# Kernel tuning notes

Measured on AMD Instinct MI355X. Metric: run time of the kernel, lower is better.

The kernel has to match this reference:

```python
import jax, jax.numpy as jnp
import numpy as np

B, S, D = 4, 2048, 1024
E, K, I = 8, 2, 2752  # num_experts, top_k, intermediate_size (64*ceil(1024*8/3/64))


def setup_inputs() -> dict:
    key = jax.random.key(0)
    k0, k1, k2, k3, k4 = jax.random.split(key, 5)
    return {
        "x": jax.random.normal(k0, (B, S, D), jnp.float32),
        "router_w": jax.random.normal(k1, (D, E), jnp.float32) * 0.02,   # gate Linear, no bias
        "w_gate": jax.random.normal(k2, (E, D, I), jnp.float32) * 0.02,  # per-expert gate proj
        "w_up": jax.random.normal(k3, (E, D, I), jnp.float32) * 0.02,    # per-expert up proj
        "w_down": jax.random.normal(k4, (E, I, D), jnp.float32) * 0.02,  # per-expert down proj
    }


def reference(x, router_w, w_gate, w_up, w_down):
    orig_shape = x.shape
    d = orig_shape[-1]
    xf = x.reshape(-1, d)                      # [T, D]
    T = xf.shape[0]
    n_experts = router_w.shape[1]

    # Router: softmax over all experts, then top-k and renormalize (matches torch order).
    probs = jax.nn.softmax(xf @ router_w, axis=-1)        # [T, E]
    w, idx = jax.lax.top_k(probs, K)                       # [T, K]
    w = w / (jnp.sum(w, axis=-1, keepdims=True) + 1e-6)

    # Dense combine weights: combine[t, e] = routing weight of expert e for token t (0 if unrouted).
    combine = jnp.zeros((T, n_experts), xf.dtype).at[jnp.arange(T)[:, None], idx].add(w)

    # Per-expert GatedMLP (SwiGLU, no bias, dropout=0 in eval): Down(SiLU(Gate(x)) * Up(x)).
    out = jnp.zeros_like(xf)
    for e in range(n_experts):  # fixed small expert count; data dims stay vectorized
        h = jax.nn.silu(xf @ w_gate[e]) * (xf @ w_up[e])   # [T, I]
        out = out + combine[:, e:e + 1] * (h @ w_down[e])  # scatter-combine
    return out.reshape(orig_shape)
```

## Files before the change

kernel.cpp:

```cpp
#include <hip/hip_runtime.h>
#include <hip/hip_bf16.h>
#include <math.h>

#define T_TOKENS 8192
#define D_MODEL  1024
#define N_EXP    8
#define I_RAW    2752
#define I_PAD    2816
#define N_CAT    5632
#define MAXROWS  18432
#define NYT      72
#define DUMP_SID (2 * T_TOKENS)

typedef __attribute__((ext_vector_type(8))) short bf16x8;
typedef __attribute__((ext_vector_type(8))) unsigned short ushort8;
typedef __attribute__((ext_vector_type(4))) float f32x4;
typedef unsigned short ushort_t;

#define CTRL_COUNT 0
#define CTRL_CUR   8
#define CTRL_SEG   16
#define CTRL_YT    32

#define VMW(n)  asm volatile("s_waitcnt vmcnt(" n ")" ::: "memory")
#define BARRIER() asm volatile("s_barrier" ::: "memory")

__device__ __forceinline__ void gll16(const void* g, void* l) {
  __builtin_amdgcn_global_load_lds(
      (const __attribute__((address_space(1))) void*)g,
      (__attribute__((address_space(3))) void*)l, 16, 0, 0);
}

__device__ __forceinline__ float silu_mul(float g, float u) {
  return g / (1.f + __expf(-g)) * u;
}

__device__ __forceinline__ float bf2f(ushort_t u) {
  return __uint_as_float((unsigned)u << 16);
}

__global__ void __launch_bounds__(64) router_kernel(
    const float* __restrict__ x, const float* __restrict__ rw,
    int* __restrict__ topidx, float* __restrict__ topw,
    __hip_bfloat16* __restrict__ xb) {
  const int t = blockIdx.x;
  const int lane = threadIdx.x;
  const float4* xr4 = (const float4*)(x + (size_t)t * D_MODEL);
  __hip_bfloat16* xbr = xb + (size_t)t * D_MODEL;
  float acc[N_EXP];
#pragma unroll
  for (int e = 0; e < N_EXP; ++e) acc[e] = 0.f;
#pragma unroll
  for (int i = 0; i < 4; ++i) {
    const int f4 = i * 64 + lane;
    const float4 v = xr4[f4];
    const int d0 = f4 * 4;
    const float* r = rw + (size_t)d0 * N_EXP;
#pragma unroll
    for (int e = 0; e < N_EXP; ++e)
      acc[e] = fmaf(v.x, r[e], fmaf(v.y, r[N_EXP + e],
               fmaf(v.z, r[2 * N_EXP + e], fmaf(v.w, r[3 * N_EXP + e], acc[e]))));
    __hip_bfloat16 b0 = __float2bfloat16(v.x), b1 = __float2bfloat16(v.y);
    __hip_bfloat16 b2 = __float2bfloat16(v.z), b3 = __float2bfloat16(v.w);
    ushort4 o;
    o.x = *(ushort_t*)&b0; o.y = *(ushort_t*)&b1;
    o.z = *(ushort_t*)&b2; o.w = *(ushort_t*)&b3;
    *(ushort4*)&xbr[d0] = o;
  }
#pragma unroll
  for (int e = 0; e < N_EXP; ++e) {
    for (int off = 32; off > 0; off >>= 1) acc[e] += __shfl_xor(acc[e], off, 64);
  }
  if (lane == 0) {
    float m = acc[0];
#pragma unroll
    for (int e = 1; e < N_EXP; ++e) m = fmaxf(m, acc[e]);
    float p[N_EXP], s = 0.f;
#pragma unroll
    for (int e = 0; e < N_EXP; ++e) { p[e] = expf(acc[e] - m); s += p[e]; }
    int i0 = 0; float v0 = p[0];
#pragma unroll
    for (int e = 1; e < N_EXP; ++e) if (p[e] > v0) { v0 = p[e]; i0 = e; }
    int i1 = -1; float v1 = -1.f;
#pragma unroll
    for (int e = 0; e < N_EXP; ++e) if (e != i0 && p[e] > v1) { v1 = p[e]; i1 = e; }
    v0 /= s; v1 /= s;
    const float r = v0 + v1 + 1e-6f;
    v0 /= r; v1 /= r;
    topidx[t * 2] = i0; topidx[t * 2 + 1] = i1;
    topw[t * 2] = v0;  topw[t * 2 + 1] = v1;
  }
}

__global__ void __launch_bounds__(512) hist_kernel(
    const int* __restrict__ topidx, int* __restrict__ ctrl) {
  __shared__ int lh[N_EXP];
  const int tid = threadIdx.x;
  if (tid < N_EXP) lh[tid] = 0;
  __syncthreads();
  const int g = blockIdx.x * 512 + tid;
  atomicAdd(&lh[topidx[g]], 1);
  __syncthreads();
  if (tid < N_EXP) atomicAdd(&ctrl[CTRL_COUNT + tid], lh[tid]);
}

__global__ void __launch_bounds__(256) transpose_cvt_kernel(
    const float* __restrict__ in, __hip_bfloat16* __restrict__ out,
    int Rin, int Cin, int Co, long in_es, long out_es, int mode) {
  __shared__ float tile[64][65];
  const float* inp = in + (size_t)blockIdx.z * in_es;
  __hip_bfloat16* outp = out + (size_t)blockIdx.z * out_es;
  const int b0 = blockIdx.x * 64;
  const int a0 = blockIdx.y * 64;
  const int tid = threadIdx.x;
  const bool inb = (b0 < Rin) && (a0 < Cin);
  const int bi0 = tid >> 4, a4 = (tid & 15) * 4;
  if (inb) {
#pragma unroll
    for (int i = 0; i < 4; ++i) {
      const int bi = bi0 + i * 16;
      const float4 v = *(const float4*)&inp[(size_t)(b0 + bi) * Cin + a0 + a4];
      tile[bi][a4] = v.x; tile[bi][a4 + 1] = v.y;
      tile[bi][a4 + 2] = v.z; tile[bi][a4 + 3] = v.w;
    }
  } else {
#pragma unroll
    for (int i = 0; i < 4; ++i) {
      const int bi = bi0 + i * 16;
      tile[bi][a4] = 0.f; tile[bi][a4 + 1] = 0.f;
      tile[bi][a4 + 2] = 0.f; tile[bi][a4 + 3] = 0.f;
    }
  }
  __syncthreads();
#pragma unroll
  for (int half = 0; half < 2; ++half) {
    const int g = tid + half * 256;
    const int al = g >> 3, bc = (g & 7) * 8;
    ushort8 o;
#pragma unroll
    for (int j = 0; j < 8; ++j) {
      __hip_bfloat16 h = __float2bfloat16(tile[bc + j][al]);
      o[j] = *(const ushort_t*)&h;
    }
    const int a = a0 + al;
    int A;
    if (mode == 0) A = a;
    else A = ((a >> 5) << 6) + ((mode == 2) ? 32 : 0) + (a & 31);
    *(ushort8*)&outp[(size_t)A * Co + b0 + bc] = o;
  }
}

__global__ void padfill_kernel(int* __restrict__ rowmap, float* __restrict__ roww) {
  const int i = blockIdx.x * blockDim.x + threadIdx.x;
  if (i < MAXROWS) { rowmap[i] = DUMP_SID; roww[i] = 0.f; }
}

__global__ void scan_kernel(int* __restrict__ ctrl) {
  if (threadIdx.x == 0 && blockIdx.x == 0) {
    int s = 0, yt = 0;
    ctrl[CTRL_SEG] = 0;
    for (int e = 0; e < N_EXP; ++e) {
      const int c = ctrl[CTRL_COUNT + e];
      const int padded = (c + 255) & ~255;
      const int n = padded >> 8;
      for (int j = 0; j < n; ++j) ctrl[CTRL_YT + yt + j] = e;
      yt += n;
      s += padded;
      ctrl[CTRL_SEG + 1 + e] = s;
    }
    for (; yt < NYT; ++yt) ctrl[CTRL_YT + yt] = -1;
  }
}

__global__ void __launch_bounds__(512) scatter_kernel(
    const int* __restrict__ topidx, const float* __restrict__ topw,
    int* __restrict__ ctrl, int* __restrict__ rowmap,
    float* __restrict__ roww) {
  __shared__ int lh[N_EXP];
  __shared__ int lbase[N_EXP];
  const int tid = threadIdx.x;
  if (tid < N_EXP) lh[tid] = 0;
  __syncthreads();
  const int g = blockIdx.x * 512 + tid;
  const int e = topidx[g];
  const int rank = atomicAdd(&lh[e], 1);
  __syncthreads();
  if (tid < N_EXP) lbase[tid] = atomicAdd(&ctrl[CTRL_CUR + tid], lh[tid]);
  __syncthreads();
  const int pos = ctrl[CTRL_SEG + e] + lbase[e] + rank;
  rowmap[pos] = g;
  roww[pos] = topw[g];
}

__global__ void __launch_bounds__(512, 2) gemm1_kernel(
    const __hip_bfloat16* __restrict__ xb,
    const __hip_bfloat16* __restrict__ wcat,
    __hip_bfloat16* __restrict__ H,
    const int* __restrict__ rowmap, const float* __restrict__ roww,
    const int* __restrict__ ctrl) {
  const unsigned b = blockIdx.x;
  const int xcd = b & 7;
  const unsigned w = b >> 3;
  const int yt = xcd * 9 + (int)(w % 9);
  const int xn = (int)(w / 9);
  const int e = ctrl[CTRL_YT + yt];
  if (e < 0) return;
  const int row0 = yt * 256;
  const int nbase = xn * 256;
  const int tid = threadIdx.x, lane = tid & 63, wid = tid >> 6;
  const int wrm = (wid >> 2) * 128, wrn = (wid & 3) * 64;

  __shared__ __align__(16) __hip_bfloat16 sA[2][2][8192];
  __shared__ __align__(16) __hip_bfloat16 sB[2][2][8192];
  __shared__ float sW[256];

  if (tid < 256) sW[tid] = roww[row0 + tid];

  const int srow = tid >> 2;
  const int kc = ((tid & 3) - ((tid >> 3) & 3)) & 3;
  int tok0 = rowmap[row0 + srow] >> 1;
  int tok1 = rowmap[row0 + 128 + srow] >> 1;
  tok0 = min(tok0, T_TOKENS - 1);
  tok1 = min(tok1, T_TOKENS - 1);
  const __hip_bfloat16* gA0 = xb + (size_t)tok0 * D_MODEL + kc * 8;
  const __hip_bfloat16* gA1 = xb + (size_t)tok1 * D_MODEL + kc * 8;
  const __hip_bfloat16* gB0 = wcat + ((size_t)e * N_CAT + nbase + srow) * D_MODEL + kc * 8;
  const __hip_bfloat16* gB1 = gB0 + (size_t)128 * D_MODEL;

  __syncthreads();

  auto stageA = [&](int sl_, int kh, int kt) {
    const int ko = kt * 64 + kh * 32;
    gll16(gA0 + ko, &sA[sl_][kh][tid * 8]);
    gll16(gA1 + ko, &sA[sl_][kh][4096 + tid * 8]);
  };
  auto stageB = [&](int sl_, int kh, int kt) {
    const int ko = kt * 64 + kh * 32;
    gll16(gB0 + ko, &sB[sl_][kh][tid * 8]);
    gll16(gB1 + ko, &sB[sl_][kh][4096 + tid * 8]);
  };

  f32x4 acc[8][4];
  const f32x4 z4 = {0.f, 0.f, 0.f, 0.f};
#pragma unroll
  for (int a_ = 0; a_ < 8; ++a_)
#pragma unroll
    for (int b_ = 0; b_ < 4; ++b_) acc[a_][b_] = z4;

  const int poff = ((lane >> 4) + ((lane & 15) >> 1)) & 3;
  const int arow = (wrm + (lane & 15)) * 32 + poff * 8;
  const int brow = (wrn + (lane & 15)) * 32 + poff * 8;

  const int NT = D_MODEL / 64;
  stageA(0, 0, 0); stageB(0, 0, 0);
  stageA(0, 1, 0); stageB(0, 1, 0);
  stageA(1, 0, 1); stageB(1, 0, 1);

#define G1_PHASE(SL, KH, STG)                                                  \
  {                                                                            \
    VMW("8");                                                                  \
    BARRIER();                                                                 \
    bf16x8 af[8], bfv[4];                                                      \
    _Pragma("unroll")                                                          \
    for (int mi = 0; mi < 8; ++mi)                                             \
      af[mi] = *(const bf16x8*)&sA[SL][KH][arow + mi * 512];                   \
    _Pragma("unroll")                                                          \
    for (int ni = 0; ni < 4; ++ni)                                             \
      bfv[ni] = *(const bf16x8*)&sB[SL][KH][brow + ni * 512];                  \
    STG;                                                                       \
    __builtin_amdgcn_s_setprio(1);                                             \
    _Pragma("unroll")                                                          \
    for (int mi = 0; mi < 8; ++mi)                                             \
      _Pragma("unroll")                                                        \
      for (int ni = 0; ni < 4; ++ni)                                           \
        acc[mi][ni] = __builtin_amdgcn_mfma_f32_16x16x32_bf16(af[mi], bfv[ni], acc[mi][ni], 0, 0, 0); \
    __builtin_amdgcn_s_setprio(0);                                             \
    BARRIER();                                                                 \
  }

#define G1_KTILE(SL, T)                                                        \
  {                                                                            \
    const int tn1 = ((T) + 1 < NT) ? (T) + 1 : 0;                              \
    const int tn2 = ((T) + 2 < NT) ? (T) + 2 : 0;                              \
    G1_PHASE(SL, 0, stageA(1 - (SL), 1, tn1); stageB(1 - (SL), 1, tn1))        \
    G1_PHASE(SL, 1, stageA((SL), 0, tn2);     stageB((SL), 0, tn2))            \
  }

  for (int t = 0; t < NT; t += 2) {
    G1_KTILE(0, t)
    G1_KTILE(1, t + 1)
  }
  VMW("0");

  const int hcolbase = ((nbase + wrn) >> 6) * 32;
#pragma unroll
  for (int mi = 0; mi < 8; ++mi) {
    const int r0 = wrm + mi * 16 + ((lane >> 4) * 4);
#pragma unroll
    for (int ni = 0; ni < 2; ++ni) {
      const int hcol = hcolbase + ni * 16 + (lane & 15);
      const f32x4 g = acc[mi][ni], u = acc[mi][ni + 2];
#pragma unroll
      for (int j = 0; j < 4; ++j) {
        const float h = silu_mul(g[j], u[j]) * sW[r0 + j];
        H[(size_t)(row0 + r0 + j) * I_PAD + hcol] = __float2bfloat16(h);
      }
    }
  }
}

__global__ void __launch_bounds__(256, 4) gemm2_kernel(
    const __hip_bfloat16* __restrict__ H,
    const __hip_bfloat16* __restrict__ wdt,
    ushort_t* __restrict__ slot,
    const int* __restrict__ rowmap, const int* __restrict__ ctrl) {
  const unsigned b = blockIdx.x;
  const int xcd = b & 7;
  const unsigned w = b >> 3;
  const int mt = xcd * 18 + (int)(w % 18);
  const int xn = (int)(w / 18);
  const int e = ctrl[CTRL_YT + (mt >> 1)];
  if (e < 0) return;
  const int row0 = mt * 128;
  const int nbase = xn * 128;
  const int tid = threadIdx.x, lane = tid & 63, wid = tid >> 6;
  const int wr = (wid >> 1) * 64, wc = (wid & 1) * 64;

  __shared__ __align__(16) __hip_bfloat16 sA[128 * 64];
  __shared__ __align__(16) __hip_bfloat16 sB[128 * 64];
  __shared__ int sTok[128];

  if (tid < 128) sTok[tid] = rowmap[row0 + tid];

  const __hip_bfloat16* gA[4];
  const __hip_bfloat16* gB[4];
#pragma unroll
  for (int i = 0; i < 4; ++i) {
    const int c = i * 256 + tid;
    const int row = c >> 3;
    const int kc8 = ((c & 7) - row) & 7;
    gA[i] = H + (size_t)(row0 + row) * I_PAD + kc8 * 8;
    gB[i] = wdt + ((size_t)e * D_MODEL + nbase + row) * I_PAD + kc8 * 8;
  }

  f32x4 acc[4][4];
  const f32x4 z4 = {0.f, 0.f, 0.f, 0.f};
#pragma unroll
  for (int a_ = 0; a_ < 4; ++a_)
#pragma unroll
    for (int b_ = 0; b_ < 4; ++b_) acc[a_][b_] = z4;

  const int NT = I_PAD / 64;
  for (int kt = 0; kt < NT; ++kt) {
    __syncthreads();
#pragma unroll
    for (int i = 0; i < 4; ++i) {
      const int c = i * 256 + tid;
      gll16(gA[i] + kt * 64, &sA[c * 8]);
      gll16(gB[i] + kt * 64, &sB[c * 8]);
    }
    __syncthreads();
#pragma unroll
    for (int ks = 0; ks < 2; ++ks) {
      bf16x8 a[4], bb[4];
#pragma unroll
      for (int mi = 0; mi < 4; ++mi) {
        const int row = wr + mi * 16 + (lane & 15);
        const int p = (ks * 4 + (lane >> 4) + row) & 7;
        a[mi] = *(const bf16x8*)&sA[row * 64 + p * 8];
      }
#pragma unroll
      for (int ni = 0; ni < 4; ++ni) {
        const int row = wc + ni * 16 + (lane & 15);
        const int p = (ks * 4 + (lane >> 4) + row) & 7;
        bb[ni] = *(const bf16x8*)&sB[row * 64 + p * 8];
      }
      __builtin_amdgcn_s_setprio(1);
#pragma unroll
      for (int mi = 0; mi < 4; ++mi)
#pragma unroll
        for (int ni = 0; ni < 4; ++ni)
          acc[mi][ni] = __builtin_amdgcn_mfma_f32_16x16x32_bf16(a[mi], bb[ni], acc[mi][ni], 0, 0, 0);
      __builtin_amdgcn_s_setprio(0);
    }
  }

#pragma unroll
  for (int mi = 0; mi < 4; ++mi) {
    const int r0 = wr + mi * 16 + ((lane >> 4) * 4);
#pragma unroll
    for (int ni = 0; ni < 4; ++ni) {
      const int col = nbase + wc + ni * 16 + (lane & 15);
#pragma unroll
      for (int j = 0; j < 4; ++j) {
        const int sid = sTok[r0 + j];
        __hip_bfloat16 hv = __float2bfloat16(acc[mi][ni][j]);
        slot[(size_t)sid * D_MODEL + col] = *(const ushort_t*)&hv;
      }
    }
  }
}

__global__ void __launch_bounds__(256) combine_kernel(
    const ushort_t* __restrict__ slot, float* __restrict__ out) {
  const int i = blockIdx.x * 256 + threadIdx.x;
  const int t = i >> 7;
  const int c = (i & 127) << 3;
  const size_t b0 = ((size_t)(t << 1)) * D_MODEL + c;
  const ushort8 a = *(const ushort8*)&slot[b0];
  const ushort8 b = *(const ushort8*)&slot[b0 + D_MODEL];
  float4 o0, o1;
  o0.x = bf2f(a[0]) + bf2f(b[0]); o0.y = bf2f(a[1]) + bf2f(b[1]);
  o0.z = bf2f(a[2]) + bf2f(b[2]); o0.w = bf2f(a[3]) + bf2f(b[3]);
  o1.x = bf2f(a[4]) + bf2f(b[4]); o1.y = bf2f(a[5]) + bf2f(b[5]);
  o1.z = bf2f(a[6]) + bf2f(b[6]); o1.w = bf2f(a[7]) + bf2f(b[7]);
  ((float4*)out)[i * 2] = o0;
  ((float4*)out)[i * 2 + 1] = o1;
}

extern "C" void kernel_launch(void* const* d_in, const int* in_sizes, int n_in,
                              void* d_out, int out_size, void* d_ws, size_t ws_size,
                              hipStream_t stream) {
  (void)in_sizes; (void)n_in; (void)ws_size; (void)out_size;
  const float* x  = (const float*)d_in[0];
  const float* rw = (const float*)d_in[1];
  const float* wg = (const float*)d_in[2];
  const float* wu = (const float*)d_in[3];
  const float* wd = (const float*)d_in[4];
  float* out = (float*)d_out;

  char* ws = (char*)d_ws;
  size_t off = 0;
  auto alloc = [&](size_t bytes) -> char* {
    char* p = ws + off;
    off += (bytes + 255) & ~(size_t)255;
    return p;
  };

  int*   ctrl   = (int*)alloc(512);
  int*   topidx = (int*)alloc((size_t)T_TOKENS * 2 * 4);
  float* topw   = (float*)alloc((size_t)T_TOKENS * 2 * 4);
  int*   rowmap = (int*)alloc((size_t)MAXROWS * 4);
  float* roww   = (float*)alloc((size_t)MAXROWS * 4);
  __hip_bfloat16* xb   = (__hip_bfloat16*)alloc((size_t)T_TOKENS * D_MODEL * 2);
  __hip_bfloat16* wcat = (__hip_bfloat16*)alloc((size_t)N_EXP * N_CAT * D_MODEL * 2);
  __hip_bfloat16* Hbuf = (__hip_bfloat16*)alloc((size_t)MAXROWS * I_PAD * 2);
  ushort_t* slotout = (ushort_t*)alloc((size_t)(2 * T_TOKENS + 1) * D_MODEL * 2);
  __hip_bfloat16* wdt = wcat;

  hipMemsetAsync(ctrl, 0, 512, stream);

  transpose_cvt_kernel<<<dim3(D_MODEL / 64, I_PAD / 64, N_EXP), 256, 0, stream>>>(
      wg, wcat, D_MODEL, I_RAW, D_MODEL, (long)D_MODEL * I_RAW, (long)N_CAT * D_MODEL, 1);
  transpose_cvt_kernel<<<dim3(D_MODEL / 64, I_PAD / 64, N_EXP), 256, 0, stream>>>(
      wu, wcat, D_MODEL, I_RAW, D_MODEL, (long)D_MODEL * I_RAW, (long)N_CAT * D_MODEL, 2);

  router_kernel<<<T_TOKENS, 64, 0, stream>>>(x, rw, topidx, topw, xb);
  hist_kernel<<<(2 * T_TOKENS) / 512, 512, 0, stream>>>(topidx, ctrl);
  padfill_kernel<<<(MAXROWS + 255) / 256, 256, 0, stream>>>(rowmap, roww);
  scan_kernel<<<1, 64, 0, stream>>>(ctrl);
  scatter_kernel<<<(2 * T_TOKENS) / 512, 512, 0, stream>>>(topidx, topw, ctrl, rowmap, roww);

  gemm1_kernel<<<dim3(NYT * 22), 512, 0, stream>>>(
      xb, wcat, Hbuf, rowmap, roww, ctrl);

  transpose_cvt_kernel<<<dim3(I_PAD / 64, D_MODEL / 64, N_EXP), 256, 0, stream>>>(
      wd, wdt, I_RAW, D_MODEL, I_PAD, (long)I_RAW * D_MODEL, (long)D_MODEL * I_PAD, 0);

  gemm2_kernel<<<dim3(NYT * 2 * 8), 256, 0, stream>>>(
      Hbuf, wdt, slotout, rowmap, ctrl);

  combine_kernel<<<(T_TOKENS * D_MODEL / 8) / 256, 256, 0, stream>>>(slotout, out);
}
```

Baseline: 520.5 us.

## Double-buffer gemm2 LDS tiles with async prefetch and drop trailing gemm1 barrier

Rewrites the down-projection GEMM main loop to use two 32-wide K slices in LDS. The global-to-LDS load for tile k+2 is issued right after the current fragments are read into registers, so loads overlap the MFMA work. This replaces the old load-sync-compute pattern that ran two __syncthreads per 64-wide tile with no overlap. It also removes the trailing barrier in the gemm1 phase macro, which relies on the next phase's barrier for correctness. The cost is a halved K step (more iterations and barriers per tile) and a wrap-around dummy prefetch at the end.

```diff
diff --git a/kernel.cpp b/kernel.cpp
--- a/kernel.cpp
+++ b/kernel.cpp
@@ -23,6 +23,7 @@
 #define CTRL_YT    32
 
 #define VMW(n)  asm volatile("s_waitcnt vmcnt(" n ")" ::: "memory")
+#define LKW0()  asm volatile("s_waitcnt lgkmcnt(0)" ::: "memory")
 #define BARRIER() asm volatile("s_barrier" ::: "memory")
 
 __device__ __forceinline__ void gll16(const void* g, void* l) {
@@ -275,7 +276,6 @@
       for (int ni = 0; ni < 4; ++ni)                                           \
         acc[mi][ni] = __builtin_amdgcn_mfma_f32_16x16x32_bf16(af[mi], bfv[ni], acc[mi][ni], 0, 0, 0); \
     __builtin_amdgcn_s_setprio(0);                                             \
-    BARRIER();                                                                 \
   }
 
 #define G1_KTILE(SL, T)                                                        \
@@ -326,22 +326,28 @@
   const int tid = threadIdx.x, lane = tid & 63, wid = tid >> 6;
   const int wr = (wid >> 1) * 64, wc = (wid & 1) * 64;
 
-  __shared__ __align__(16) __hip_bfloat16 sA[128 * 64];
-  __shared__ __align__(16) __hip_bfloat16 sB[128 * 64];
+  __shared__ __align__(16) __hip_bfloat16 sA[2][4096];
+  __shared__ __align__(16) __hip_bfloat16 sB[2][4096];
   __shared__ int sTok[128];
 
   if (tid < 128) sTok[tid] = rowmap[row0 + tid];
 
-  const __hip_bfloat16* gA[4];
-  const __hip_bfloat16* gB[4];
-#pragma unroll
-  for (int i = 0; i < 4; ++i) {
-    const int c = i * 256 + tid;
-    const int row = c >> 3;
-    const int kc8 = ((c & 7) - row) & 7;
-    gA[i] = H + (size_t)(row0 + row) * I_PAD + kc8 * 8;
-    gB[i] = wdt + ((size_t)e * D_MODEL + nbase + row) * I_PAD + kc8 * 8;
-  }
+  const int r0s = tid >> 2;
+  const int kc = ((tid & 3) - ((tid >> 3) & 3)) & 3;
+  const __hip_bfloat16* gA0 = H + (size_t)(row0 + r0s) * I_PAD + kc * 8;
+  const __hip_bfloat16* gA1 = gA0 + (size_t)64 * I_PAD;
+  const __hip_bfloat16* gB0 = wdt + ((size_t)e * D_MODEL + nbase + r0s) * I_PAD + kc * 8;
+  const __hip_bfloat16* gB1 = gB0 + (size_t)64 * I_PAD;
+
+  __syncthreads();
+
+  auto stage = [&](int sl, int kt) {
+    const int ko = kt * 32;
+    gll16(gA0 + ko, &sA[sl][tid * 8]);
+    gll16(gA1 + ko, &sA[sl][2048 + tid * 8]);
+    gll16(gB0 + ko, &sB[sl][tid * 8]);
+    gll16(gB1 + ko, &sB[sl][2048 + tid * 8]);
+  };
 
   f32x4 acc[4][4];
   const f32x4 z4 = {0.f, 0.f, 0.f, 0.f};
@@ -350,40 +356,37 @@
 #pragma unroll
     for (int b_ = 0; b_ < 4; ++b_) acc[a_][b_] = z4;
 
-  const int NT = I_PAD / 64;
+  const int poff = ((lane >> 4) + ((lane & 15) >> 1)) & 3;
+  const int aoff = (wr + (lane & 15)) * 32 + poff * 8;
+  const int boff = (wc + (lane & 15)) * 32 + poff * 8;
+
+  const int NT = I_PAD / 32;
+  stage(0, 0); stage(1, 1);
+
   for (int kt = 0; kt < NT; ++kt) {
-    __syncthreads();
-#pragma unroll
-    for (int i = 0; i < 4; ++i) {
-      const int c = i * 256 + tid;
-      gll16(gA[i] + kt * 64, &sA[c * 8]);
-      gll16(gB[i] + kt * 64, &sB[c * 8]);
-    }
-    __syncthreads();
-#pragma unroll
-    for (int ks = 0; ks < 2; ++ks) {
-      bf16x8 a[4], bb[4];
-#pragma unroll
-      for (int mi = 0; mi < 4; ++mi) {
-        const int row = wr + mi * 16 + (lane & 15);
-        const int p = (ks * 4 + (lane >> 4) + row) & 7;
-        a[mi] = *(const bf16x8*)&sA[row * 64 + p * 8];
-      }
-#pragma unroll
-      for (int ni = 0; ni < 4; ++ni) {
-        const int row = wc + ni * 16 + (lane & 15);
-        const int p = (ks * 4 + (lane >> 4) + row) & 7;
-        bb[ni] = *(const bf16x8*)&sB[row * 64 + p * 8];
-      }
-      __builtin_amdgcn_s_setprio(1);
-#pragma unroll
-      for (int mi = 0; mi < 4; ++mi)
-#pragma unroll
-        for (int ni = 0; ni < 4; ++ni)
-          acc[mi][ni] = __builtin_amdgcn_mfma_f32_16x16x32_bf16(a[mi], bb[ni], acc[mi][ni], 0, 0, 0);
-      __builtin_amdgcn_s_setprio(0);
-    }
-  }
+    const int sl = kt & 1;
+    VMW("4");
+    BARRIER();
+    bf16x8 a[4], bb[4];
+#pragma unroll
+    for (int mi = 0; mi < 4; ++mi)
+      a[mi] = *(const bf16x8*)&sA[sl][aoff + mi * 512];
+#pragma unroll
+    for (int ni = 0; ni < 4; ++ni)
+      bb[ni] = *(const bf16x8*)&sB[sl][boff + ni * 512];
+    LKW0();
+    BARRIER();
+    const int ktn = (kt + 2 < NT) ? kt + 2 : 0;
+    stage(sl, ktn);
+    __builtin_amdgcn_s_setprio(1);
+#pragma unroll
+    for (int mi = 0; mi < 4; ++mi)
+#pragma unroll
+      for (int ni = 0; ni < 4; ++ni)
+        acc[mi][ni] = __builtin_amdgcn_mfma_f32_16x16x32_bf16(a[mi], bb[ni], acc[mi][ni], 0, 0, 0);
+    __builtin_amdgcn_s_setprio(0);
+  }
+  VMW("0");
 
 #pragma unroll
   for (int mi = 0; mi < 4; ++mi) {
```

After: 522.7 us. No clear change (+0.4%).
